# Kernel optimization log

Measured on AMD Instinct MI355X. Metric: run time of the kernel, lower is better.

## Reference

```python
import jax, jax.numpy as jnp
import numpy as np

N_NODES = 50000
N_EDGES = 1600000
D_IN = 64
D_HID = 64
N_CLASSES = 10
N_GRAPHS = 64


def setup_inputs() -> dict:
    key = jax.random.key(0)
    ks = jax.random.split(key, 9)
    x = jax.random.normal(ks[0], (N_NODES, D_IN), dtype=jnp.float32)
    edge_index = jax.random.randint(ks[1], (2, N_EDGES), 0, N_NODES, dtype=jnp.int64)
    batch = jnp.sort(jax.random.randint(ks[2], (N_NODES,), 0, N_GRAPHS, dtype=jnp.int64))
    s1 = 1.0 / np.sqrt(D_IN)
    s2 = 1.0 / np.sqrt(D_HID)
    W1 = jax.random.uniform(ks[3], (D_IN, D_HID), jnp.float32, -s1, s1)
    b1 = jnp.zeros((D_HID,), jnp.float32)
    W2 = jax.random.uniform(ks[4], (D_HID, D_HID), jnp.float32, -s2, s2)
    b2 = jnp.zeros((D_HID,), jnp.float32)
    Wfc = jax.random.uniform(ks[5], (D_HID, N_CLASSES), jnp.float32, -s2, s2)
    bfc = jnp.zeros((N_CLASSES,), jnp.float32)
    return {"x": x, "edge_index": edge_index, "batch": batch,
            "W1": W1, "b1": b1, "W2": W2, "b2": b2, "Wfc": Wfc, "bfc": bfc}


def _gcn_conv(h, src, dst, deg_inv_sqrt, W, b):
    # h: [N, d_in] -> linear then normalized scatter-add aggregation (PyG GCNConv)
    h = h @ W                                   # [N, d_out]
    norm = deg_inv_sqrt[src] * deg_inv_sqrt[dst]  # [E+N]
    msg = h[src] * norm[:, None]                # gather + scale  [E+N, d_out]
    out = jax.ops.segment_sum(msg, dst, num_segments=h.shape[0])
    return out + b


def reference(x, edge_index, batch, W1, b1, W2, b2, Wfc, bfc):
    n = x.shape[0]
    loops = jnp.arange(n, dtype=edge_index.dtype)
    src = jnp.concatenate([edge_index[0], loops])  # self-loops appended
    dst = jnp.concatenate([edge_index[1], loops])
    deg = jax.ops.segment_sum(jnp.ones_like(dst, x.dtype), dst, num_segments=n)
    deg_inv_sqrt = jnp.where(deg > 0, jax.lax.rsqrt(deg), 0.0)

    h = jax.nn.relu(_gcn_conv(x, src, dst, deg_inv_sqrt, W1, b1))
    # dropout is identity in eval mode
    h = jax.nn.relu(_gcn_conv(h, src, dst, deg_inv_sqrt, W2, b2))

    # global mean pool over graphs
    sums = jax.ops.segment_sum(h, batch, num_segments=N_GRAPHS)      # [G, d]
    cnts = jax.ops.segment_sum(jnp.ones((n,), h.dtype), batch, num_segments=N_GRAPHS)
    pooled = sums / jnp.maximum(cnts, 1.0)[:, None]
    return pooled @ Wfc + bfc                                        # [G, classes]
```

## Files before the change

kernel.cpp:

```cpp
#include <hip/hip_runtime.h>
#include <hip/hip_bf16.h>

#define PART_T 8192
#define PTHREADS 1024
#define NF_PAD 1024
#define BCAP 2560
#define CAPN 80
#define GS 32

__device__ __forceinline__ bool detect_f64_block(const unsigned* __restrict__ raw,
                                                 int nelem, int* nz, int t) {
    if (t == 0) *nz = 0;
    __syncthreads();
    int found = 0;
    int lim = nelem < 2048 ? nelem : 2048;
#pragma unroll
    for (int k = 0; k < 8; k++) {
        int i = t * 8 + k;
        if (i < lim) found |= (raw[2 * i + 1] != 0u);
    }
    if (found) atomicOr(nz, 1);
    __syncthreads();
    return (*nz) == 0;
}

__device__ __forceinline__ float bf_lo(unsigned u) { return __uint_as_float(u << 16); }
__device__ __forceinline__ float bf_hi(unsigned u) { return __uint_as_float(u & 0xFFFF0000u); }
__device__ __forceinline__ unsigned short f2bf(float f) {
    __hip_bfloat16 h = __float2bfloat16(f);
    unsigned short u;
    __builtin_memcpy(&u, &h, 2);
    return u;
}
__device__ __forceinline__ unsigned pack2bf(float a, float b) {
    return (unsigned)f2bf(a) | ((unsigned)f2bf(b) << 16);
}

__global__ __launch_bounds__(PTHREADS) void partition_edges(const int* __restrict__ raw, int E,
                                                            int NF, int* __restrict__ gcur,
                                                            unsigned* __restrict__ elist) {
    __shared__ int cnt[NF_PAD];
    __shared__ int pfx[NF_PAD];
    __shared__ int gbase[NF_PAD];
    __shared__ int wsum[PTHREADS / 64];
    __shared__ unsigned stage[PART_T];
    __shared__ int nz;
    int t = threadIdx.x;
    bool f64 = detect_f64_block((const unsigned*)raw, 2 * E, &nz, t);
    long long base = (long long)blockIdx.x * PART_T;
    int tileN = (int)min((long long)PART_T, (long long)E - base);

    cnt[t] = 0;
    __syncthreads();

    unsigned pk[PART_T / PTHREADS];
#pragma unroll
    for (int k = 0; k < PART_T / PTHREADS; k++) {
        long long e = base + k * PTHREADS + t;
        if (e < (long long)E) {
            int s = f64 ? raw[2 * e] : raw[e];
            int d = f64 ? raw[2 * ((long long)E + e)] : raw[E + e];
            unsigned p = (unsigned)s | ((unsigned)d << 16);
            pk[k] = p;
            atomicAdd(&cnt[d >> 6], 1);
        } else {
            pk[k] = 0xFFFFFFFFu;
        }
    }
    __syncthreads();

    int a = cnt[t];
    int lane = t & 63;
    int incl = a;
#pragma unroll
    for (int o = 1; o < 64; o <<= 1) {
        int y = __shfl_up(incl, o, 64);
        if (lane >= o) incl += y;
    }
    if (lane == 63) wsum[t >> 6] = incl;
    __syncthreads();
    int wpre = 0;
    int wid = t >> 6;
    for (int wwi = 0; wwi < wid; wwi++) wpre += wsum[wwi];
    pfx[t] = wpre + incl - a;

    if (t < NF) {
        gbase[t] = (a > 0) ? (t * BCAP + atomicAdd(&gcur[t * GS], a)) : 0;
    }
    __syncthreads();
    cnt[t] = 0;
    __syncthreads();

#pragma unroll
    for (int k = 0; k < PART_T / PTHREADS; k++) {
        long long e = base + k * PTHREADS + t;
        if (e < (long long)E) {
            unsigned p = pk[k];
            int f = p >> 22;
            int r = atomicAdd(&cnt[f], 1);
            stage[pfx[f] + r] = p;
        }
    }
    __syncthreads();

    for (int i = t; i < tileN; i += PTHREADS) {
        unsigned v = stage[i];
        int f = v >> 22;
        elist[gbase[f] + (i - pfx[f])] = v;
    }
}

__global__ __launch_bounds__(256) void bucket_csr(const unsigned* __restrict__ elist,
                                                  const int* __restrict__ gcur,
                                                  int n,
                                                  unsigned short* __restrict__ ssrc,
                                                  int* __restrict__ deg,
                                                  float* __restrict__ dis) {
    __shared__ int cnt[64];
    int b = blockIdx.x;
    int t = threadIdx.x;
    int beg = b * BCAP, end = beg + gcur[b * GS];
    if (t < 64) cnt[t] = 0;
    __syncthreads();
    for (int e = beg + t; e < end; e += 256) {
        unsigned v = elist[e];
        int local = (v >> 16) & 63;
        int r = atomicAdd(&cnt[local], 1);
        if (r < CAPN)
            ssrc[(long long)(b * 64 + local) * CAPN + r] = (unsigned short)(v & 0xFFFFu);
    }
    __syncthreads();
    if (t < 64) {
        int node = b * 64 + t;
        if (node < n) {
            int d = cnt[t];
            deg[node] = d;
            dis[node] = rsqrtf((float)(d + 1));
        }
    }
}

__global__ __launch_bounds__(256) void linear64_f32(const float* __restrict__ in,
                                                    const float* __restrict__ W,
                                                    const float* __restrict__ dis,
                                                    __hip_bfloat16* __restrict__ outH, int n) {
    __shared__ float sIn[64][64];
    int t = threadIdx.x;
    int ln = t >> 6, od = t & 63;
    float w[64];
#pragma unroll
    for (int k = 0; k < 64; k++) w[k] = W[k * 64 + od];
    int base = blockIdx.x * 64;
    long long ebase = (long long)base * 64;
    long long etot = (long long)n * 64;
#pragma unroll
    for (int pass = 0; pass < 16; pass++) {
        long long idx = ebase + pass * 256 + t;
        sIn[(pass * 256 + t) >> 6][(pass * 256 + t) & 63] = (idx < etot) ? in[idx] : 0.f;
    }
    __syncthreads();
    for (int pass = 0; pass < 16; pass++) {
        int node = base + pass * 4 + ln;
        if (node < n) {
            float acc = 0.f;
            const float4* row = (const float4*)sIn[pass * 4 + ln];
#pragma unroll
            for (int k = 0; k < 16; k++) {
                float4 sv = row[k];
                acc += sv.x * w[4 * k] + sv.y * w[4 * k + 1] + sv.z * w[4 * k + 2] + sv.w * w[4 * k + 3];
            }
            outH[(long long)node * 64 + od] = __float2bfloat16(acc * dis[node]);
        }
    }
}

__global__ __launch_bounds__(256) void linear64_bf16(const unsigned short* __restrict__ inH,
                                                     const float* __restrict__ W,
                                                     const float* __restrict__ dis,
                                                     __hip_bfloat16* __restrict__ outH, int n) {
    __shared__ float sIn[64][64];
    int t = threadIdx.x;
    int ln = t >> 6, od = t & 63;
    float w[64];
#pragma unroll
    for (int k = 0; k < 64; k++) w[k] = W[k * 64 + od];
    int base = blockIdx.x * 64;
    long long ebase2 = (long long)base * 32;
    long long etot2 = ((long long)n * 64) >> 1;
#pragma unroll
    for (int pass = 0; pass < 8; pass++) {
        int li = pass * 256 + t;
        long long idx = ebase2 + li;
        unsigned u = (idx < etot2) ? ((const unsigned*)inH)[idx] : 0u;
        sIn[(2 * li) >> 6][(2 * li) & 63] = bf_lo(u);
        sIn[(2 * li) >> 6][(2 * li + 1) & 63] = bf_hi(u);
    }
    __syncthreads();
    for (int pass = 0; pass < 16; pass++) {
        int node = base + pass * 4 + ln;
        if (node < n) {
            float acc = 0.f;
            const float4* row = (const float4*)sIn[pass * 4 + ln];
#pragma unroll
            for (int k = 0; k < 16; k++) {
                float4 sv = row[k];
                acc += sv.x * w[4 * k] + sv.y * w[4 * k + 1] + sv.z * w[4 * k + 2] + sv.w * w[4 * k + 3];
            }
            outH[(long long)node * 64 + od] = __float2bfloat16(acc * dis[node]);
        }
    }
}

template <int K>
__device__ __forceinline__ void gather_chunks(const unsigned short* __restrict__ hs,
                                              const unsigned short* __restrict__ ssrc,
                                              long long beg, int g, int l, int d,
                                              float& a0, float& a1, float& a2, float& a3,
                                              float& a4, float& a5, float& a6, float& a7) {
    int idx[K];
#pragma unroll
    for (int k = 0; k < K; k++) idx[k] = (int)ssrc[beg + g + 8 * k];
#pragma unroll
    for (int k = 0; k < K; k++) {
        uint4 v = ((const uint4*)(hs + (long long)idx[k] * 64))[l];
        if (g + 8 * k >= d) { v.x = 0u; v.y = 0u; v.z = 0u; v.w = 0u; }
        a0 += bf_lo(v.x); a1 += bf_hi(v.x);
        a2 += bf_lo(v.y); a3 += bf_hi(v.y);
        a4 += bf_lo(v.z); a5 += bf_hi(v.z);
        a6 += bf_lo(v.w); a7 += bf_hi(v.w);
    }
}

__global__ __launch_bounds__(256) void gather_agg(const unsigned short* __restrict__ hs,
                                                  const int* __restrict__ deg,
                                                  const unsigned short* __restrict__ ssrc,
                                                  const float* __restrict__ dis,
                                                  const float* __restrict__ bias,
                                                  __hip_bfloat16* __restrict__ outH, int n) {
    int t = threadIdx.x;
    int lane = t & 63;
    int g = lane >> 3;
    int l = lane & 7;
    int node = blockIdx.x * 4 + (t >> 6);
    if (node >= n) return;
    long long beg = (long long)node * CAPN;
    int d = deg[node];
    float a0 = 0.f, a1 = 0.f, a2 = 0.f, a3 = 0.f, a4 = 0.f, a5 = 0.f, a6 = 0.f, a7 = 0.f;

    if (d <= 32) {
        gather_chunks<4>(hs, ssrc, beg, g, l, d, a0, a1, a2, a3, a4, a5, a6, a7);
    } else if (d <= 40) {
        gather_chunks<5>(hs, ssrc, beg, g, l, d, a0, a1, a2, a3, a4, a5, a6, a7);
    } else if (d <= 48) {
        gather_chunks<6>(hs, ssrc, beg, g, l, d, a0, a1, a2, a3, a4, a5, a6, a7);
    } else {
        gather_chunks<8>(hs, ssrc, beg, g, l, d, a0, a1, a2, a3, a4, a5, a6, a7);
        for (int i = 64 + g; i < d; i += 8) {
            int s = (int)ssrc[beg + i];
            uint4 v = ((const uint4*)(hs + (long long)s * 64))[l];
            a0 += bf_lo(v.x); a1 += bf_hi(v.x);
            a2 += bf_lo(v.y); a3 += bf_hi(v.y);
            a4 += bf_lo(v.z); a5 += bf_hi(v.z);
            a6 += bf_lo(v.w); a7 += bf_hi(v.w);
        }
    }
    if (g == 0) {
        uint4 v = ((const uint4*)(hs + (long long)node * 64))[l];
        a0 += bf_lo(v.x); a1 += bf_hi(v.x);
        a2 += bf_lo(v.y); a3 += bf_hi(v.y);
        a4 += bf_lo(v.z); a5 += bf_hi(v.z);
        a6 += bf_lo(v.w); a7 += bf_hi(v.w);
    }
#pragma unroll
    for (int o = 8; o <= 32; o <<= 1) {
        a0 += __shfl_xor(a0, o, 64);
        a1 += __shfl_xor(a1, o, 64);
        a2 += __shfl_xor(a2, o, 64);
        a3 += __shfl_xor(a3, o, 64);
        a4 += __shfl_xor(a4, o, 64);
        a5 += __shfl_xor(a5, o, 64);
        a6 += __shfl_xor(a6, o, 64);
        a7 += __shfl_xor(a7, o, 64);
    }
    if (g == 0) {
        float dv = dis[node];
        const float4* bp = (const float4*)bias;
        float4 b0 = bp[2 * l], b1 = bp[2 * l + 1];
        float r0 = dv * a0 + b0.x; r0 = r0 > 0.f ? r0 : 0.f;
        float r1 = dv * a1 + b0.y; r1 = r1 > 0.f ? r1 : 0.f;
        float r2 = dv * a2 + b0.z; r2 = r2 > 0.f ? r2 : 0.f;
        float r3 = dv * a3 + b0.w; r3 = r3 > 0.f ? r3 : 0.f;
        float r4 = dv * a4 + b1.x; r4 = r4 > 0.f ? r4 : 0.f;
        float r5 = dv * a5 + b1.y; r5 = r5 > 0.f ? r5 : 0.f;
        float r6 = dv * a6 + b1.z; r6 = r6 > 0.f ? r6 : 0.f;
        float r7 = dv * a7 + b1.w; r7 = r7 > 0.f ? r7 : 0.f;
        uint4 o4;
        o4.x = pack2bf(r0, r1);
        o4.y = pack2bf(r2, r3);
        o4.z = pack2bf(r4, r5);
        o4.w = pack2bf(r6, r7);
        ((uint4*)(outH + (long long)node * 64))[l] = o4;
    }
}

__global__ __launch_bounds__(256) void pool_sum(const unsigned short* __restrict__ h2,
                                                const int* __restrict__ braw,
                                                float* __restrict__ psum,
                                                int* __restrict__ pcnt, int n) {
    __shared__ int nz;
    int t = threadIdx.x;
    bool f64 = detect_f64_block((const unsigned*)braw, n, &nz, t);
    int lane = t & 63;
    int base = (blockIdx.x * 4 + (t >> 6)) * 32;
    float acc = 0.f;
    int g = -1, cnt = 0;
    for (int i = 0; i < 32; i++) {
        int node = base + i;
        if (node >= n) break;
        int bg = f64 ? braw[2 * node] : braw[node];
        if (bg != g) {
            if (g >= 0) {
                atomicAdd(&psum[g * 64 + lane], acc);
                if (lane == 0) atomicAdd(&pcnt[g], cnt);
            }
            g = bg; acc = 0.f; cnt = 0;
        }
        unsigned short u = h2[(long long)node * 64 + lane];
        acc += __uint_as_float((unsigned)u << 16);
        cnt++;
    }
    if (g >= 0) {
        atomicAdd(&psum[g * 64 + lane], acc);
        if (lane == 0) atomicAdd(&pcnt[g], cnt);
    }
}

__global__ __launch_bounds__(640) void final_fc(const float* __restrict__ psum,
                                                const int* __restrict__ pcnt,
                                                const float* __restrict__ Wfc,
                                                const float* __restrict__ bfc,
                                                float* __restrict__ out) {
    __shared__ float sP[64 * 64];
    __shared__ float sW[64 * 10];
    int t = threadIdx.x;
    for (int i = t; i < 4096; i += 640) sP[i] = psum[i];
    if (t < 640) sW[t] = Wfc[t];
    __syncthreads();
    int g = t / 10, c = t % 10;
    float acc = 0.f;
#pragma unroll
    for (int k = 0; k < 64; k++) acc += sP[g * 64 + k] * sW[k * 10 + c];
    float cnt = (float)pcnt[g];
    if (cnt < 1.f) cnt = 1.f;
    out[g * 10 + c] = acc / cnt + bfc[c];
}

static inline int cdiv(long long a, int b) { return (int)((a + b - 1) / b); }

extern "C" void kernel_launch(void* const* d_in, const int* in_sizes, int n_in,
                              void* d_out, int out_size, void* d_ws, size_t ws_size,
                              hipStream_t stream) {
    const float* x    = (const float*)d_in[0];
    const int*   eraw = (const int*)d_in[1];
    const int*   braw = (const int*)d_in[2];
    const float* W1   = (const float*)d_in[3];
    const float* b1   = (const float*)d_in[4];
    const float* W2   = (const float*)d_in[5];
    const float* b2   = (const float*)d_in[6];
    const float* Wfc  = (const float*)d_in[7];
    const float* bfc  = (const float*)d_in[8];
    float* out = (float*)d_out;

    const int N  = in_sizes[0] / 64;
    const int E  = in_sizes[1] / 2;
    const int NF = cdiv(N, 64);

    char* p = (char*)d_ws;
    auto carve = [&](size_t bytes) { char* q = p; p += (bytes + 255) / 256 * 256; return q; };
    unsigned*       elist = (unsigned*)carve(((size_t)NF + 1) * BCAP * sizeof(unsigned));
    unsigned short* ssrc  = (unsigned short*)carve((size_t)(NF + 1) * 64 * CAPN * sizeof(unsigned short));
    size_t ssrc_bytes = (size_t)(NF + 1) * 64 * CAPN * sizeof(unsigned short);
    char* zbeg = p;
    int*            gcur  = (int*)carve((size_t)NF * GS * sizeof(int));
    float*          psum  = (float*)carve(64 * 64 * sizeof(float));
    int*            pcnt  = (int*)carve(64 * sizeof(int));
    size_t zlen = (size_t)(p - zbeg);
    int*            deg   = (int*)carve((size_t)N * sizeof(int));
    float*          dis   = (float*)carve((size_t)N * sizeof(float));
    __hip_bfloat16* hs    = (__hip_bfloat16*)carve((size_t)N * 64 * sizeof(__hip_bfloat16));
    __hip_bfloat16* h1    = (__hip_bfloat16*)carve((size_t)N * 64 * sizeof(__hip_bfloat16));
    __hip_bfloat16* h2    = (__hip_bfloat16*)carve((size_t)N * 64 * sizeof(__hip_bfloat16));
    (void)carve(4 << 20);

    hipMemsetAsync(zbeg, 0, zlen, stream);
    hipMemsetAsync(ssrc, 0, ssrc_bytes, stream);

    partition_edges<<<cdiv(E, PART_T), PTHREADS, 0, stream>>>(eraw, E, NF, gcur, elist);
    bucket_csr<<<NF, 256, 0, stream>>>(elist, gcur, N, ssrc, deg, dis);

    linear64_f32<<<cdiv(N, 64), 256, 0, stream>>>(x, W1, dis, hs, N);
    gather_agg<<<cdiv(N, 4), 256, 0, stream>>>((const unsigned short*)hs, deg, ssrc, dis, b1, h1, N);

    linear64_bf16<<<cdiv(N, 64), 256, 0, stream>>>((const unsigned short*)h1, W2, dis, hs, N);
    gather_agg<<<cdiv(N, 4), 256, 0, stream>>>((const unsigned short*)hs, deg, ssrc, dis, b2, h2, N);

    pool_sum<<<cdiv(N, 128), 256, 0, stream>>>((const unsigned short*)h2, braw, psum, pcnt, N);
    final_fc<<<1, 640, 0, stream>>>(psum, pcnt, Wfc, bfc, out);
}
```

Baseline: 227.5 us.

## Fuse layer-1 aggregation with layer-2 linear and aggregation with pooling and FC

Layer-1 gather-aggregate now writes its rows into LDS and the layer-2 linear transform runs in the same kernel, so the h1 round trip through global memory disappears. Layer-2 aggregation is fused with mean pooling, and a last-block-done counter runs the final FC inside that kernel. The ssrc memset is also dropped. In exchange each block gathers 64 nodes serially across 4 waves, which may lower memory-level parallelism relative to the old 4-nodes-per-block gather, and correctness now depends on the masked gather never reading unwritten ssrc slots.

```diff
diff --git a/kernel.cpp b/kernel.cpp
--- a/kernel.cpp
+++ b/kernel.cpp
@@ -1,5 +1,6 @@
 #include <hip/hip_runtime.h>
 #include <hip/hip_bf16.h>
+
 
 #define PART_T 8192
 #define PTHREADS 1024
@@ -31,9 +32,6 @@
     unsigned short u;
     __builtin_memcpy(&u, &h, 2);
     return u;
-}
-__device__ __forceinline__ unsigned pack2bf(float a, float b) {
-    return (unsigned)f2bf(a) | ((unsigned)f2bf(b) << 16);
 }
 
 __global__ __launch_bounds__(PTHREADS) void partition_edges(const int* __restrict__ raw, int E,
@@ -143,7 +141,7 @@
 __global__ __launch_bounds__(256) void linear64_f32(const float* __restrict__ in,
                                                     const float* __restrict__ W,
                                                     const float* __restrict__ dis,
-                                                    __hip_bfloat16* __restrict__ outH, int n) {
+                                                    unsigned short* __restrict__ outH, int n) {
     __shared__ float sIn[64][64];
     int t = threadIdx.x;
     int ln = t >> 6, od = t & 63;
@@ -169,50 +167,13 @@
                 float4 sv = row[k];
                 acc += sv.x * w[4 * k] + sv.y * w[4 * k + 1] + sv.z * w[4 * k + 2] + sv.w * w[4 * k + 3];
             }
-            outH[(long long)node * 64 + od] = __float2bfloat16(acc * dis[node]);
-        }
-    }
-}
-
-__global__ __launch_bounds__(256) void linear64_bf16(const unsigned short* __restrict__ inH,
-                                                     const float* __restrict__ W,
-                                                     const float* __restrict__ dis,
-                                                     __hip_bfloat16* __restrict__ outH, int n) {
-    __shared__ float sIn[64][64];
-    int t = threadIdx.x;
-    int ln = t >> 6, od = t & 63;
-    float w[64];
-#pragma unroll
-    for (int k = 0; k < 64; k++) w[k] = W[k * 64 + od];
-    int base = blockIdx.x * 64;
-    long long ebase2 = (long long)base * 32;
-    long long etot2 = ((long long)n * 64) >> 1;
-#pragma unroll
-    for (int pass = 0; pass < 8; pass++) {
-        int li = pass * 256 + t;
-        long long idx = ebase2 + li;
-        unsigned u = (idx < etot2) ? ((const unsigned*)inH)[idx] : 0u;
-        sIn[(2 * li) >> 6][(2 * li) & 63] = bf_lo(u);
-        sIn[(2 * li) >> 6][(2 * li + 1) & 63] = bf_hi(u);
-    }
-    __syncthreads();
-    for (int pass = 0; pass < 16; pass++) {
-        int node = base + pass * 4 + ln;
-        if (node < n) {
-            float acc = 0.f;
-            const float4* row = (const float4*)sIn[pass * 4 + ln];
-#pragma unroll
-            for (int k = 0; k < 16; k++) {
-                float4 sv = row[k];
-                acc += sv.x * w[4 * k] + sv.y * w[4 * k + 1] + sv.z * w[4 * k + 2] + sv.w * w[4 * k + 3];
-            }
-            outH[(long long)node * 64 + od] = __float2bfloat16(acc * dis[node]);
+            outH[(long long)node * 64 + od] = f2bf(acc * dis[node]);
         }
     }
 }
 
 template <int K>
-__device__ __forceinline__ void gather_chunks(const unsigned short* __restrict__ hs,
+__device__ __forceinline__ void gather_chunks(const unsigned short* __restrict__ hsrc,
                                               const unsigned short* __restrict__ ssrc,
                                               long long beg, int g, int l, int d,
                                               float& a0, float& a1, float& a2, float& a3,
@@ -222,7 +183,7 @@
     for (int k = 0; k < K; k++) idx[k] = (int)ssrc[beg + g + 8 * k];
 #pragma unroll
     for (int k = 0; k < K; k++) {
-        uint4 v = ((const uint4*)(hs + (long long)idx[k] * 64))[l];
+        uint4 v = ((const uint4*)(hsrc + (long long)idx[k] * 64))[l];
         if (g + 8 * k >= d) { v.x = 0u; v.y = 0u; v.z = 0u; v.w = 0u; }
         a0 += bf_lo(v.x); a1 += bf_hi(v.x);
         a2 += bf_lo(v.y); a3 += bf_hi(v.y);
@@ -231,33 +192,28 @@
     }
 }
 
-__global__ __launch_bounds__(256) void gather_agg(const unsigned short* __restrict__ hs,
-                                                  const int* __restrict__ deg,
-                                                  const unsigned short* __restrict__ ssrc,
-                                                  const float* __restrict__ dis,
-                                                  const float* __restrict__ bias,
-                                                  __hip_bfloat16* __restrict__ outH, int n) {
-    int t = threadIdx.x;
-    int lane = t & 63;
-    int g = lane >> 3;
-    int l = lane & 7;
-    int node = blockIdx.x * 4 + (t >> 6);
-    if (node >= n) return;
+__device__ __forceinline__ void gather_node_to_lds(const unsigned short* __restrict__ hsrc,
+                                                   const int* __restrict__ deg,
+                                                   const unsigned short* __restrict__ ssrc,
+                                                   const float* __restrict__ dis,
+                                                   const float* __restrict__ bias,
+                                                   int node, int g, int l,
+                                                   float* __restrict__ ldsRow) {
     long long beg = (long long)node * CAPN;
     int d = deg[node];
     float a0 = 0.f, a1 = 0.f, a2 = 0.f, a3 = 0.f, a4 = 0.f, a5 = 0.f, a6 = 0.f, a7 = 0.f;
 
     if (d <= 32) {
-        gather_chunks<4>(hs, ssrc, beg, g, l, d, a0, a1, a2, a3, a4, a5, a6, a7);
+        gather_chunks<4>(hsrc, ssrc, beg, g, l, d, a0, a1, a2, a3, a4, a5, a6, a7);
     } else if (d <= 40) {
-        gather_chunks<5>(hs, ssrc, beg, g, l, d, a0, a1, a2, a3, a4, a5, a6, a7);
+        gather_chunks<5>(hsrc, ssrc, beg, g, l, d, a0, a1, a2, a3, a4, a5, a6, a7);
     } else if (d <= 48) {
-        gather_chunks<6>(hs, ssrc, beg, g, l, d, a0, a1, a2, a3, a4, a5, a6, a7);
+        gather_chunks<6>(hsrc, ssrc, beg, g, l, d, a0, a1, a2, a3, a4, a5, a6, a7);
     } else {
-        gather_chunks<8>(hs, ssrc, beg, g, l, d, a0, a1, a2, a3, a4, a5, a6, a7);
+        gather_chunks<8>(hsrc, ssrc, beg, g, l, d, a0, a1, a2, a3, a4, a5, a6, a7);
         for (int i = 64 + g; i < d; i += 8) {
             int s = (int)ssrc[beg + i];
-            uint4 v = ((const uint4*)(hs + (long long)s * 64))[l];
+            uint4 v = ((const uint4*)(hsrc + (long long)s * 64))[l];
             a0 += bf_lo(v.x); a1 += bf_hi(v.x);
             a2 += bf_lo(v.y); a3 += bf_hi(v.y);
             a4 += bf_lo(v.z); a5 += bf_hi(v.z);
@@ -265,7 +221,7 @@
         }
     }
     if (g == 0) {
-        uint4 v = ((const uint4*)(hs + (long long)node * 64))[l];
+        uint4 v = ((const uint4*)(hsrc + (long long)node * 64))[l];
         a0 += bf_lo(v.x); a1 += bf_hi(v.x);
         a2 += bf_lo(v.y); a3 += bf_hi(v.y);
         a4 += bf_lo(v.z); a5 += bf_hi(v.z);
@@ -294,65 +250,129 @@
         float r5 = dv * a5 + b1.y; r5 = r5 > 0.f ? r5 : 0.f;
         float r6 = dv * a6 + b1.z; r6 = r6 > 0.f ? r6 : 0.f;
         float r7 = dv * a7 + b1.w; r7 = r7 > 0.f ? r7 : 0.f;
-        uint4 o4;
-        o4.x = pack2bf(r0, r1);
-        o4.y = pack2bf(r2, r3);
-        o4.z = pack2bf(r4, r5);
-        o4.w = pack2bf(r6, r7);
-        ((uint4*)(outH + (long long)node * 64))[l] = o4;
-    }
-}
-
-__global__ __launch_bounds__(256) void pool_sum(const unsigned short* __restrict__ h2,
-                                                const int* __restrict__ braw,
-                                                float* __restrict__ psum,
-                                                int* __restrict__ pcnt, int n) {
-    __shared__ int nz;
+        float4* q = (float4*)(ldsRow + 8 * l);
+        q[0] = make_float4(r0, r1, r2, r3);
+        q[1] = make_float4(r4, r5, r6, r7);
+    }
+}
+
+__global__ __launch_bounds__(256) void gather1_lin2(const unsigned short* __restrict__ hs,
+                                                    const int* __restrict__ deg,
+                                                    const unsigned short* __restrict__ ssrc,
+                                                    const float* __restrict__ dis,
+                                                    const float* __restrict__ b1,
+                                                    const float* __restrict__ W2,
+                                                    unsigned short* __restrict__ hs2, int n) {
+    __shared__ float sIn[64][64];
     int t = threadIdx.x;
-    bool f64 = detect_f64_block((const unsigned*)braw, n, &nz, t);
-    int lane = t & 63;
-    int base = (blockIdx.x * 4 + (t >> 6)) * 32;
-    float acc = 0.f;
-    int g = -1, cnt = 0;
-    for (int i = 0; i < 32; i++) {
-        int node = base + i;
-        if (node >= n) break;
-        int bg = f64 ? braw[2 * node] : braw[node];
-        if (bg != g) {
-            if (g >= 0) {
-                atomicAdd(&psum[g * 64 + lane], acc);
-                if (lane == 0) atomicAdd(&pcnt[g], cnt);
+    int lane = t & 63, wv = t >> 6;
+    int g = lane >> 3, l = lane & 7;
+    int base = blockIdx.x * 64;
+
+    for (int i = 0; i < 16; i++) {
+        int local = wv + 4 * i;
+        int node = base + local;
+        if (node < n)
+            gather_node_to_lds(hs, deg, ssrc, dis, b1, node, g, l, sIn[local]);
+    }
+    __syncthreads();
+
+    int od = lane, ln = wv;
+    float w[64];
+#pragma unroll
+    for (int k = 0; k < 64; k++) w[k] = W2[k * 64 + od];
+    for (int pass = 0; pass < 16; pass++) {
+        int node = base + pass * 4 + ln;
+        if (node < n) {
+            float acc = 0.f;
+            const float4* row = (const float4*)sIn[pass * 4 + ln];
+#pragma unroll
+            for (int k = 0; k < 16; k++) {
+                float4 sv = row[k];
+                acc += sv.x * w[4 * k] + sv.y * w[4 * k + 1] + sv.z * w[4 * k + 2] + sv.w * w[4 * k + 3];
             }
-            g = bg; acc = 0.f; cnt = 0;
-        }
-        unsigned short u = h2[(long long)node * 64 + lane];
-        acc += __uint_as_float((unsigned)u << 16);
-        cnt++;
-    }
-    if (g >= 0) {
-        atomicAdd(&psum[g * 64 + lane], acc);
-        if (lane == 0) atomicAdd(&pcnt[g], cnt);
-    }
-}
-
-__global__ __launch_bounds__(640) void final_fc(const float* __restrict__ psum,
-                                                const int* __restrict__ pcnt,
-                                                const float* __restrict__ Wfc,
-                                                const float* __restrict__ bfc,
-                                                float* __restrict__ out) {
-    __shared__ float sP[64 * 64];
-    __shared__ float sW[64 * 10];
+            hs2[(long long)node * 64 + od] = f2bf(acc * dis[node]);
+        }
+    }
+}
+
+__global__ __launch_bounds__(256) void gather2_pool_fc(const unsigned short* __restrict__ hs2,
+                                                       const int* __restrict__ deg,
+                                                       const unsigned short* __restrict__ ssrc,
+                                                       const float* __restrict__ dis,
+                                                       const float* __restrict__ b2,
+                                                       const int* __restrict__ braw,
+                                                       float* __restrict__ psum,
+                                                       int* __restrict__ pcnt,
+                                                       int* __restrict__ done,
+                                                       const float* __restrict__ Wfc,
+                                                       const float* __restrict__ bfc,
+                                                       float* __restrict__ out, int n) {
+    __shared__ float sH[64][64];
+    __shared__ float sW[640];
+    __shared__ int s_nz;
+    __shared__ int s_last;
     int t = threadIdx.x;
-    for (int i = t; i < 4096; i += 640) sP[i] = psum[i];
-    if (t < 640) sW[t] = Wfc[t];
-    __syncthreads();
-    int g = t / 10, c = t % 10;
-    float acc = 0.f;
-#pragma unroll
-    for (int k = 0; k < 64; k++) acc += sP[g * 64 + k] * sW[k * 10 + c];
-    float cnt = (float)pcnt[g];
-    if (cnt < 1.f) cnt = 1.f;
-    out[g * 10 + c] = acc / cnt + bfc[c];
+    int lane = t & 63, wv = t >> 6;
+    int g = lane >> 3, l = lane & 7;
+    int base = blockIdx.x * 64;
+
+    bool f64b = detect_f64_block((const unsigned*)braw, n, &s_nz, t);
+
+    for (int i = 0; i < 16; i++) {
+        int local = wv + 4 * i;
+        int node = base + local;
+        if (node < n)
+            gather_node_to_lds(hs2, deg, ssrc, dis, b2, node, g, l, sH[local]);
+    }
+    __syncthreads();
+
+    {
+        float acc = 0.f;
+        int gseg = -1, cnt = 0;
+        for (int i = 0; i < 16; i++) {
+            int local = wv * 16 + i;
+            int node = base + local;
+            if (node >= n) break;
+            int bg = f64b ? braw[2 * node] : braw[node];
+            if (bg != gseg) {
+                if (gseg >= 0) {
+                    atomicAdd(&psum[gseg * 64 + lane], acc);
+                    if (lane == 0) atomicAdd(&pcnt[gseg], cnt);
+                }
+                gseg = bg; acc = 0.f; cnt = 0;
+            }
+            acc += sH[local][lane];
+            cnt++;
+        }
+        if (gseg >= 0) {
+            atomicAdd(&psum[gseg * 64 + lane], acc);
+            if (lane == 0) atomicAdd(&pcnt[gseg], cnt);
+        }
+    }
+
+    __threadfence();
+    __syncthreads();
+    if (t == 0) s_last = (atomicAdd(done, 1) == (int)gridDim.x - 1);
+    __syncthreads();
+    if (s_last) {
+        __threadfence();
+        float* sP = (float*)sH;
+        for (int i = t; i < 4096; i += 256)
+            sP[i] = __hip_atomic_load(&psum[i], __ATOMIC_RELAXED, __HIP_MEMORY_SCOPE_AGENT);
+        for (int i = t; i < 640; i += 256) sW[i] = Wfc[i];
+        __syncthreads();
+        for (int i = t; i < 640; i += 256) {
+            int gg = i / 10, c = i % 10;
+            float acc = 0.f;
+#pragma unroll
+            for (int k = 0; k < 64; k++) acc += sP[gg * 64 + k] * sW[k * 10 + c];
+            int craw = __hip_atomic_load(&pcnt[gg], __ATOMIC_RELAXED, __HIP_MEMORY_SCOPE_AGENT);
+            float cc = (float)craw;
+            if (cc < 1.f) cc = 1.f;
+            out[i] = acc / cc + bfc[c];
+        }
+    }
 }
 
 static inline int cdiv(long long a, int b) { return (int)((a + b - 1) / b); }
@@ -379,31 +399,25 @@
     auto carve = [&](size_t bytes) { char* q = p; p += (bytes + 255) / 256 * 256; return q; };
     unsigned*       elist = (unsigned*)carve(((size_t)NF + 1) * BCAP * sizeof(unsigned));
     unsigned short* ssrc  = (unsigned short*)carve((size_t)(NF + 1) * 64 * CAPN * sizeof(unsigned short));
-    size_t ssrc_bytes = (size_t)(NF + 1) * 64 * CAPN * sizeof(unsigned short);
     char* zbeg = p;
     int*            gcur  = (int*)carve((size_t)NF * GS * sizeof(int));
     float*          psum  = (float*)carve(64 * 64 * sizeof(float));
     int*            pcnt  = (int*)carve(64 * sizeof(int));
+    int*            done  = (int*)carve(256);
     size_t zlen = (size_t)(p - zbeg);
     int*            deg   = (int*)carve((size_t)N * sizeof(int));
     float*          dis   = (float*)carve((size_t)N * sizeof(float));
-    __hip_bfloat16* hs    = (__hip_bfloat16*)carve((size_t)N * 64 * sizeof(__hip_bfloat16));
-    __hip_bfloat16* h1    = (__hip_bfloat16*)carve((size_t)N * 64 * sizeof(__hip_bfloat16));
-    __hip_bfloat16* h2    = (__hip_bfloat16*)carve((size_t)N * 64 * sizeof(__hip_bfloat16));
+    unsigned short* hs    = (unsigned short*)carve((size_t)N * 64 * sizeof(unsigned short));
+    unsigned short* hs2   = (unsigned short*)carve((size_t)N * 64 * sizeof(unsigned short));
     (void)carve(4 << 20);
 
     hipMemsetAsync(zbeg, 0, zlen, stream);
-    hipMemsetAsync(ssrc, 0, ssrc_bytes, stream);
 
     partition_edges<<<cdiv(E, PART_T), PTHREADS, 0, stream>>>(eraw, E, NF, gcur, elist);
     bucket_csr<<<NF, 256, 0, stream>>>(elist, gcur, N, ssrc, deg, dis);
 
     linear64_f32<<<cdiv(N, 64), 256, 0, stream>>>(x, W1, dis, hs, N);
-    gather_agg<<<cdiv(N, 4), 256, 0, stream>>>((const unsigned short*)hs, deg, ssrc, dis, b1, h1, N);
-
-    linear64_bf16<<<cdiv(N, 64), 256, 0, stream>>>((const unsigned short*)h1, W2, dis, hs, N);
-    gather_agg<<<cdiv(N, 4), 256, 0, stream>>>((const unsigned short*)hs, deg, ssrc, dis, b2, h2, N);
-
-    pool_sum<<<cdiv(N, 128), 256, 0, stream>>>((const unsigned short*)h2, braw, psum, pcnt, N);
-    final_fc<<<1, 640, 0, stream>>>(psum, pcnt, Wfc, bfc, out);
-}
+    gather1_lin2<<<cdiv(N, 64), 256, 0, stream>>>(hs, deg, ssrc, dis, b1, W2, hs2, N);
+    gather2_pool_fc<<<cdiv(N, 64), 256, 0, stream>>>(hs2, deg, ssrc, dis, b2, braw,
+                                                     psum, pcnt, done, Wfc, bfc, out, N);
+}
```

Result: slower. 269.6 us (+18.5%).
